# Optimization experiments

Hardware: AMD Instinct MI355X
Metric: run time of the kernel (lower is better)

The kernel has to match this reference:

```python
import jax, jax.numpy as jnp
import numpy as np

B = 131072   # batch
D = 16       # input_dim
L1 = 4       # num lattices in layer 1 (= ceil(D / DPL))
DPL = 4      # input_dim_per_lattice
E = 24       # output_size (ensemble columns)
K = 16       # calibrator keypoints per feature
NV = 2 ** DPL  # hypercube corners per lattice (lattice_keypoints=2 per dim)


def setup_inputs() -> dict:
    key = jax.random.key(0)
    k1, k2, k3, k4, k5 = jax.random.split(key, 5)
    x = jax.random.normal(k1, (B, D), jnp.float32)
    # piecewise-linear calibrators: sorted input keypoints, monotone outputs in [0,1]
    cal_kp = jnp.sort(jax.random.uniform(k2, (D, K), jnp.float32, -3.0, 3.0), axis=-1)
    raw = jax.random.uniform(k3, (D, K), jnp.float32, 0.1, 1.0)
    cv = jnp.cumsum(raw, axis=-1)
    cal_vals = (cv - cv[:, :1]) / (cv[:, -1:] - cv[:, :1])  # [D,K] in [0,1], increasing
    kernels1 = jax.random.uniform(k4, (E, L1, NV), jnp.float32)  # per-column layer-1 lattice vertices
    kernels2 = jax.random.uniform(k5, (E, 1, NV), jnp.float32)   # per-column layer-2 lattice vertices
    return {"x": x, "cal_kp": cal_kp, "cal_vals": cal_vals,
            "kernels1": kernels1, "kernels2": kernels2}


def _mlin_weights(xg):
    """Multilinear (HYPERCUBE) interpolation weights for unit lattices.
    xg: [..., L, d] with entries in [0,1]. Returns [..., L, 2^d] corner weights,
    corner index with dim 0 as most-significant bit."""
    d = xg.shape[-1]
    w = jnp.ones(xg.shape[:-1] + (1,), xg.dtype)
    for i in range(d):
        xi = xg[..., i]                              # [..., L]
        pair = jnp.stack([1.0 - xi, xi], axis=-1)    # [..., L, 2]
        w = (w[..., :, None] * pair[..., None, :]).reshape(*xg.shape[:-1], -1)
    return w


def reference(x, cal_kp, cal_vals, kernels1, kernels2):
    # 1) calibrate_and_stack: per-feature piecewise-linear calibration to [0,1]
    xc = jax.vmap(jnp.interp)(x.T, cal_kp, cal_vals).T           # [B, D]
    # 2) layer 1: split D dims into L1 lattices of DPL dims each (clip_inputs=True)
    xg1 = jnp.clip(xc.reshape(-1, L1, DPL), 0.0, 1.0)            # [B, L1, DPL]
    w1 = _mlin_weights(xg1)                                      # [B, L1, 2^DPL]
    h1 = jnp.einsum('blk,elk->ebl', w1, kernels1)                # [E, B, L1]
    # 3) layer 2: one lattice of DPL dims per ensemble column
    xg2 = jnp.clip(h1[:, :, None, :], 0.0, 1.0)                  # [E, B, 1, DPL]
    w2 = _mlin_weights(xg2)                                      # [E, B, 1, 2^DPL]
    out = jnp.einsum('eblk,elk->be', w2, kernels2)               # [B, E]
    return out
```

## Files before the change

### kernel.cpp

```cpp
#include <hip/hip_runtime.h>


typedef _Float16 f16x4 __attribute__((ext_vector_type(4)));
typedef float f32x4 __attribute__((ext_vector_type(4)));
typedef float f32x2 __attribute__((ext_vector_type(2)));

namespace {
constexpr int kD = 16, kE = 24, kK = 16, kNV = 16;
constexpr int kThreads = 256;
constexpr int kRPB = 64;
constexpr int kKpS  = 17;
constexpr int kAffS = 17;
constexpr int kWS   = 67;
constexpr int kK2S  = 20;
}

static __device__ __forceinline__ f32x2 fma2(f32x2 a, f32x2 b, f32x2 c) {
#if __has_builtin(__builtin_elementwise_fma)
    return __builtin_elementwise_fma(a, b, c);
#else
    return (f32x2){fmaf(a[0], b[0], c[0]), fmaf(a[1], b[1], c[1])};
#endif
}
static __device__ __forceinline__ f32x2 fma2s(f32x2 a, float b, float c) {
    return fma2(a, (f32x2){b, b}, (f32x2){c, c});
}
static __device__ __forceinline__ f32x2 clamp01(f32x2 v) {
    return (f32x2){fminf(fmaxf(v[0], 0.f), 1.f), fminf(fmaxf(v[1], 0.f), 1.f)};
}

__global__ __launch_bounds__(kThreads, 8) void lattice_fwd(
    const float* __restrict__ x,
    const float* __restrict__ cal_kp,
    const float* __restrict__ cal_vals,
    const float* __restrict__ k1,
    const float* __restrict__ k2,
    float* __restrict__ out)
{
    __shared__ float sKp[kD * kKpS];
    __shared__ f32x2 sAff[kD * kAffS];
    __shared__ f16x4 sW[16 * kWS];
    __shared__ f16x4 sK1[4 * 2 * 64];
    __shared__ float sK2[32 * kK2S];

    const int tid  = threadIdx.x;
    const int lane = tid & 63;
    const int wv   = __builtin_amdgcn_readfirstlane(tid >> 6);
    const int q    = lane >> 4;
    const int r15  = lane & 15;

    const int rowBase = blockIdx.x * kRPB + wv * 16;

    f32x4 xin = *reinterpret_cast<const f32x4*>(
        x + (size_t)(rowBase + r15) * kD + 4 * q);

    {
        int d = tid >> 4, k = tid & 15;
        sKp[d * kKpS + k] = (k == 15) ? __builtin_inff() : cal_kp[tid];
    }
    if (tid < kD * 15) {
        int d = tid / 15;
        int k = tid - d * 15;
        float kp0 = cal_kp[d * kK + k];
        float kp1 = cal_kp[d * kK + k + 1];
        float v0  = cal_vals[d * kK + k];
        float v1  = cal_vals[d * kK + k + 1];
        float dxv = kp1 - kp0;
        float slope = (dxv > 0.0f) ? (v1 - v0) / dxv : 0.0f;
        sAff[d * kAffS + k] = (f32x2){slope, fmaf(-slope, kp0, v0)};
    }
    #pragma unroll
    for (int s0 = 0; s0 < 2; ++s0) {
        int s  = tid + s0 * kThreads;
        int l  = s >> 7;
        int n  = (s >> 6) & 1;
        int ls = s & 63;
        int e  = n * 16 + (ls & 15);
        int g  = ls >> 4;
        f16x4 v = {(_Float16)0.f, (_Float16)0.f, (_Float16)0.f, (_Float16)0.f};
        if (e < kE) {
            const float* src = k1 + ((size_t)(e * 4 + l) * kNV + 4 * g);
            v[0] = (_Float16)src[0]; v[1] = (_Float16)src[1];
            v[2] = (_Float16)src[2]; v[3] = (_Float16)src[3];
        }
        sK1[s] = v;
    }
    {
        int e = tid >> 3, j4 = (tid >> 1) & 3, h = tid & 1;
        float a = 0.f, d = 0.f;
        if (e < kE) {
            a = k2[e * kNV + 4 * j4 + 2 * h];
            d = k2[e * kNV + 4 * j4 + 2 * h + 1] - a;
        }
        sK2[e * kK2S + 4 * j4 + h]     = a;
        sK2[e * kK2S + 4 * j4 + 2 + h] = d;
    }

    __syncthreads();

    float xc[4];
    #pragma unroll
    for (int i = 0; i < 4; ++i) {
        const int d = 4 * q + i;
        const float xv = xin[i];
        const float* kpb = &sKp[d * kKpS];
        int j = 0;
        #pragma unroll
        for (int s = 8; s >= 1; s >>= 1) {
            float kps = kpb[j + s];
            j = (xv >= kps) ? j + s : j;
        }
        f32x2 ent = sAff[d * kAffS + j];
        xc[i] = fminf(fmaxf(fmaf(ent[0], xv, ent[1]), 0.0f), 1.0f);
    }

    float wf[16];
    {
        float a = xc[0], b = xc[1], c = xc[2], d = xc[3];
        float t2[2] = {1.0f - a, a};
        float t4[4];
        #pragma unroll
        for (int j = 0; j < 2; ++j) { t4[2*j] = t2[j]*(1.0f-b); t4[2*j+1] = t2[j]*b; }
        float t8[8];
        #pragma unroll
        for (int j = 0; j < 4; ++j) { t8[2*j] = t4[j]*(1.0f-c); t8[2*j+1] = t4[j]*c; }
        #pragma unroll
        for (int j = 0; j < 8; ++j) { wf[2*j] = t8[j]*(1.0f-d); wf[2*j+1] = t8[j]*d; }
    }

    #pragma unroll
    for (int g = 0; g < 4; ++g) {
        f16x4 v;
        v[0] = (_Float16)wf[4*g+0]; v[1] = (_Float16)wf[4*g+1];
        v[2] = (_Float16)wf[4*g+2]; v[3] = (_Float16)wf[4*g+3];
        sW[(wv * 4 + q) * kWS + r15 + 16 * g] = v;
    }
    asm volatile("s_waitcnt lgkmcnt(0)" ::: "memory");

    f16x4 af[4];
    #pragma unroll
    for (int l = 0; l < 4; ++l) af[l] = sW[(wv * 4 + l) * kWS + lane];

    #pragma unroll
    for (int n = 0; n < 2; ++n) {
        const int e = n * 16 + r15;

        f32x4 acc[4];
        #pragma unroll
        for (int l = 0; l < 4; ++l) {
            f16x4 bf = sK1[(l * 2 + n) * 64 + lane];
            acc[l] = __builtin_amdgcn_mfma_f32_16x16x16f16(
                af[l], bf, (f32x4){0.f, 0.f, 0.f, 0.f}, 0, 0, 0);
        }

        f32x2 h3a = clamp01((f32x2){acc[3][0], acc[3][1]});
        f32x2 h3b = clamp01((f32x2){acc[3][2], acc[3][3]});
        f32x2 h2a = clamp01((f32x2){acc[2][0], acc[2][1]});
        f32x2 h2b = clamp01((f32x2){acc[2][2], acc[2][3]});

        f32x2 v4a[4], v4b[4];
        const float* kr = &sK2[e * kK2S];
        #pragma unroll
        for (int j4 = 0; j4 < 4; ++j4) {
            f32x4 kq = *reinterpret_cast<const f32x4*>(kr + 4 * j4);
            f32x2 a0 = fma2s(h3a, kq[2], kq[0]);
            f32x2 b0 = fma2s(h3a, kq[3], kq[1]);
            v4a[j4]  = fma2(h2a, b0 - a0, a0);
            f32x2 a1 = fma2s(h3b, kq[2], kq[0]);
            f32x2 b1 = fma2s(h3b, kq[3], kq[1]);
            v4b[j4]  = fma2(h2b, b1 - a1, a1);
        }

        #pragma unroll
        for (int p = 0; p < 2; ++p) {
            f32x2 h1 = clamp01((f32x2){acc[1][2*p], acc[1][2*p+1]});
            f32x2 h0 = clamp01((f32x2){acc[0][2*p], acc[0][2*p+1]});
            const f32x2* v4 = (p == 0) ? v4a : v4b;
            f32x2 w0 = fma2(h1, v4[1] - v4[0], v4[0]);
            f32x2 w1 = fma2(h1, v4[3] - v4[2], v4[2]);
            f32x2 o  = fma2(h0, w1 - w0, w0);
            if (e < kE) {
                size_t r0 = (size_t)(rowBase + q * 4 + 2 * p);
                out[r0 * kE + e]       = o[0];
                out[(r0 + 1) * kE + e] = o[1];
            }
        }
    }
}

extern "C" void kernel_launch(void* const* d_in, const int* in_sizes, int n_in,
                              void* d_out, int out_size, void* d_ws, size_t ws_size,
                              hipStream_t stream) {
    const float* x        = (const float*)d_in[0];
    const float* cal_kp   = (const float*)d_in[1];
    const float* cal_vals = (const float*)d_in[2];
    const float* k1       = (const float*)d_in[3];
    const float* k2       = (const float*)d_in[4];
    float* out = (float*)d_out;

    hipLaunchKernelGGL(lattice_fwd, dim3(131072 / kRPB), dim3(kThreads), 0, stream,
                       x, cal_kp, cal_vals, k1, k2, out);
}
```

Measured before the change: 14.13 us.

## Keep lattice kernels in registers and process two row tiles per block

Layer-1 MFMA B-fragments and the layer-2 vertex coefficients are now loaded straight from global memory into registers, replacing the shared-memory staging arrays. Each block also handles two 64-row tiles, prefetching the next tile's x before working on the current one, which halves the grid and amortizes the per-block setup of calibration tables. The cost is higher register pressure (launch bounds lowered to 4 waves) and fewer blocks for latency hiding.

```diff
diff --git a/kernel.cpp b/kernel.cpp
--- a/kernel.cpp
+++ b/kernel.cpp
@@ -8,11 +8,11 @@
 namespace {
 constexpr int kD = 16, kE = 24, kK = 16, kNV = 16;
 constexpr int kThreads = 256;
-constexpr int kRPB = 64;
+constexpr int kRPT = 64;
+constexpr int kTPB = 2;
 constexpr int kKpS  = 17;
 constexpr int kAffS = 17;
 constexpr int kWS   = 67;
-constexpr int kK2S  = 20;
 }
 
 static __device__ __forceinline__ f32x2 fma2(f32x2 a, f32x2 b, f32x2 c) {
@@ -29,7 +29,7 @@
     return (f32x2){fminf(fmaxf(v[0], 0.f), 1.f), fminf(fmaxf(v[1], 0.f), 1.f)};
 }
 
-__global__ __launch_bounds__(kThreads, 8) void lattice_fwd(
+__global__ __launch_bounds__(kThreads, 4) void lattice_fwd(
     const float* __restrict__ x,
     const float* __restrict__ cal_kp,
     const float* __restrict__ cal_vals,
@@ -40,19 +40,38 @@
     __shared__ float sKp[kD * kKpS];
     __shared__ f32x2 sAff[kD * kAffS];
     __shared__ f16x4 sW[16 * kWS];
-    __shared__ f16x4 sK1[4 * 2 * 64];
-    __shared__ float sK2[32 * kK2S];
 
     const int tid  = threadIdx.x;
     const int lane = tid & 63;
     const int wv   = __builtin_amdgcn_readfirstlane(tid >> 6);
     const int q    = lane >> 4;
     const int r15  = lane & 15;
-
-    const int rowBase = blockIdx.x * kRPB + wv * 16;
-
-    f32x4 xin = *reinterpret_cast<const f32x4*>(
-        x + (size_t)(rowBase + r15) * kD + 4 * q);
+    const int g    = lane >> 4;
+
+    const int eN[2]  = {r15, 16 + r15};
+    const int eLd[2] = {r15, (16 + r15 < kE) ? 16 + r15 : kE - 1};
+
+    f16x4 bf[4][2];
+    #pragma unroll
+    for (int l = 0; l < 4; ++l)
+        #pragma unroll
+        for (int n = 0; n < 2; ++n) {
+            f32x4 v = *reinterpret_cast<const f32x4*>(
+                k1 + ((size_t)(eLd[n] * 4 + l) * kNV + 4 * g));
+            f16x4 h;
+            h[0] = (_Float16)v[0]; h[1] = (_Float16)v[1];
+            h[2] = (_Float16)v[2]; h[3] = (_Float16)v[3];
+            bf[l][n] = h;
+        }
+    f32x4 kq[2][4];
+    #pragma unroll
+    for (int n = 0; n < 2; ++n)
+        #pragma unroll
+        for (int j4 = 0; j4 < 4; ++j4) {
+            f32x4 c = *reinterpret_cast<const f32x4*>(
+                k2 + (size_t)eLd[n] * kNV + 4 * j4);
+            kq[n][j4] = (f32x4){c[0], c[2], c[1] - c[0], c[3] - c[2]};
+        }
 
     {
         int d = tid >> 4, k = tid & 15;
@@ -69,120 +88,102 @@
         float slope = (dxv > 0.0f) ? (v1 - v0) / dxv : 0.0f;
         sAff[d * kAffS + k] = (f32x2){slope, fmaf(-slope, kp0, v0)};
     }
-    #pragma unroll
-    for (int s0 = 0; s0 < 2; ++s0) {
-        int s  = tid + s0 * kThreads;
-        int l  = s >> 7;
-        int n  = (s >> 6) & 1;
-        int ls = s & 63;
-        int e  = n * 16 + (ls & 15);
-        int g  = ls >> 4;
-        f16x4 v = {(_Float16)0.f, (_Float16)0.f, (_Float16)0.f, (_Float16)0.f};
-        if (e < kE) {
-            const float* src = k1 + ((size_t)(e * 4 + l) * kNV + 4 * g);
-            v[0] = (_Float16)src[0]; v[1] = (_Float16)src[1];
-            v[2] = (_Float16)src[2]; v[3] = (_Float16)src[3];
-        }
-        sK1[s] = v;
-    }
-    {
-        int e = tid >> 3, j4 = (tid >> 1) & 3, h = tid & 1;
-        float a = 0.f, d = 0.f;
-        if (e < kE) {
-            a = k2[e * kNV + 4 * j4 + 2 * h];
-            d = k2[e * kNV + 4 * j4 + 2 * h + 1] - a;
-        }
-        sK2[e * kK2S + 4 * j4 + h]     = a;
-        sK2[e * kK2S + 4 * j4 + 2 + h] = d;
-    }
 
     __syncthreads();
 
-    float xc[4];
-    #pragma unroll
-    for (int i = 0; i < 4; ++i) {
-        const int d = 4 * q + i;
-        const float xv = xin[i];
-        const float* kpb = &sKp[d * kKpS];
-        int j = 0;
-        #pragma unroll
-        for (int s = 8; s >= 1; s >>= 1) {
-            float kps = kpb[j + s];
-            j = (xv >= kps) ? j + s : j;
-        }
-        f32x2 ent = sAff[d * kAffS + j];
-        xc[i] = fminf(fmaxf(fmaf(ent[0], xv, ent[1]), 0.0f), 1.0f);
-    }
-
-    float wf[16];
-    {
-        float a = xc[0], b = xc[1], c = xc[2], d = xc[3];
-        float t2[2] = {1.0f - a, a};
-        float t4[4];
-        #pragma unroll
-        for (int j = 0; j < 2; ++j) { t4[2*j] = t2[j]*(1.0f-b); t4[2*j+1] = t2[j]*b; }
-        float t8[8];
-        #pragma unroll
-        for (int j = 0; j < 4; ++j) { t8[2*j] = t4[j]*(1.0f-c); t8[2*j+1] = t4[j]*c; }
-        #pragma unroll
-        for (int j = 0; j < 8; ++j) { wf[2*j] = t8[j]*(1.0f-d); wf[2*j+1] = t8[j]*d; }
-    }
-
-    #pragma unroll
-    for (int g = 0; g < 4; ++g) {
-        f16x4 v;
-        v[0] = (_Float16)wf[4*g+0]; v[1] = (_Float16)wf[4*g+1];
-        v[2] = (_Float16)wf[4*g+2]; v[3] = (_Float16)wf[4*g+3];
-        sW[(wv * 4 + q) * kWS + r15 + 16 * g] = v;
-    }
-    asm volatile("s_waitcnt lgkmcnt(0)" ::: "memory");
-
-    f16x4 af[4];
-    #pragma unroll
-    for (int l = 0; l < 4; ++l) af[l] = sW[(wv * 4 + l) * kWS + lane];
-
-    #pragma unroll
-    for (int n = 0; n < 2; ++n) {
-        const int e = n * 16 + r15;
-
-        f32x4 acc[4];
-        #pragma unroll
-        for (int l = 0; l < 4; ++l) {
-            f16x4 bf = sK1[(l * 2 + n) * 64 + lane];
-            acc[l] = __builtin_amdgcn_mfma_f32_16x16x16f16(
-                af[l], bf, (f32x4){0.f, 0.f, 0.f, 0.f}, 0, 0, 0);
-        }
-
-        f32x2 h3a = clamp01((f32x2){acc[3][0], acc[3][1]});
-        f32x2 h3b = clamp01((f32x2){acc[3][2], acc[3][3]});
-        f32x2 h2a = clamp01((f32x2){acc[2][0], acc[2][1]});
-        f32x2 h2b = clamp01((f32x2){acc[2][2], acc[2][3]});
-
-        f32x2 v4a[4], v4b[4];
-        const float* kr = &sK2[e * kK2S];
-        #pragma unroll
-        for (int j4 = 0; j4 < 4; ++j4) {
-            f32x4 kq = *reinterpret_cast<const f32x4*>(kr + 4 * j4);
-            f32x2 a0 = fma2s(h3a, kq[2], kq[0]);
-            f32x2 b0 = fma2s(h3a, kq[3], kq[1]);
-            v4a[j4]  = fma2(h2a, b0 - a0, a0);
-            f32x2 a1 = fma2s(h3b, kq[2], kq[0]);
-            f32x2 b1 = fma2s(h3b, kq[3], kq[1]);
-            v4b[j4]  = fma2(h2b, b1 - a1, a1);
-        }
-
-        #pragma unroll
-        for (int p = 0; p < 2; ++p) {
-            f32x2 h1 = clamp01((f32x2){acc[1][2*p], acc[1][2*p+1]});
-            f32x2 h0 = clamp01((f32x2){acc[0][2*p], acc[0][2*p+1]});
-            const f32x2* v4 = (p == 0) ? v4a : v4b;
-            f32x2 w0 = fma2(h1, v4[1] - v4[0], v4[0]);
-            f32x2 w1 = fma2(h1, v4[3] - v4[2], v4[2]);
-            f32x2 o  = fma2(h0, w1 - w0, w0);
-            if (e < kE) {
-                size_t r0 = (size_t)(rowBase + q * 4 + 2 * p);
-                out[r0 * kE + e]       = o[0];
-                out[(r0 + 1) * kE + e] = o[1];
+    const int rowTile0 = blockIdx.x * (kRPT * kTPB);
+    f32x4 xin = *reinterpret_cast<const f32x4*>(
+        x + (size_t)(rowTile0 + wv * 16 + r15) * kD + 4 * q);
+
+    for (int t = 0; t < kTPB; ++t) {
+        const int rowBase = rowTile0 + t * kRPT + wv * 16;
+        f32x4 xcur = xin;
+        if (t + 1 < kTPB)
+            xin = *reinterpret_cast<const f32x4*>(
+                x + (size_t)(rowTile0 + (t + 1) * kRPT + wv * 16 + r15) * kD + 4 * q);
+
+        float xc[4];
+        #pragma unroll
+        for (int i = 0; i < 4; ++i) {
+            const int d = 4 * q + i;
+            const float xv = xcur[i];
+            const float* kpb = &sKp[d * kKpS];
+            int j = 0;
+            #pragma unroll
+            for (int s = 8; s >= 1; s >>= 1) {
+                float kps = kpb[j + s];
+                j = (xv >= kps) ? j + s : j;
+            }
+            f32x2 ent = sAff[d * kAffS + j];
+            xc[i] = fminf(fmaxf(fmaf(ent[0], xv, ent[1]), 0.0f), 1.0f);
+        }
+
+        float wf[16];
+        {
+            float a = xc[0], b = xc[1], c = xc[2], d = xc[3];
+            float t2[2] = {1.0f - a, a};
+            float t4[4];
+            #pragma unroll
+            for (int j = 0; j < 2; ++j) { t4[2*j] = t2[j]*(1.0f-b); t4[2*j+1] = t2[j]*b; }
+            float t8[8];
+            #pragma unroll
+            for (int j = 0; j < 4; ++j) { t8[2*j] = t4[j]*(1.0f-c); t8[2*j+1] = t4[j]*c; }
+            #pragma unroll
+            for (int j = 0; j < 8; ++j) { wf[2*j] = t8[j]*(1.0f-d); wf[2*j+1] = t8[j]*d; }
+        }
+
+        #pragma unroll
+        for (int gg = 0; gg < 4; ++gg) {
+            f16x4 v;
+            v[0] = (_Float16)wf[4*gg+0]; v[1] = (_Float16)wf[4*gg+1];
+            v[2] = (_Float16)wf[4*gg+2]; v[3] = (_Float16)wf[4*gg+3];
+            sW[(wv * 4 + q) * kWS + r15 + 16 * gg] = v;
+        }
+        asm volatile("s_waitcnt lgkmcnt(0)" ::: "memory");
+
+        f16x4 af[4];
+        #pragma unroll
+        for (int l = 0; l < 4; ++l) af[l] = sW[(wv * 4 + l) * kWS + lane];
+
+        #pragma unroll
+        for (int n = 0; n < 2; ++n) {
+            f32x4 acc[4];
+            #pragma unroll
+            for (int l = 0; l < 4; ++l)
+                acc[l] = __builtin_amdgcn_mfma_f32_16x16x16f16(
+                    af[l], bf[l][n], (f32x4){0.f, 0.f, 0.f, 0.f}, 0, 0, 0);
+
+            f32x2 h3a = clamp01((f32x2){acc[3][0], acc[3][1]});
+            f32x2 h3b = clamp01((f32x2){acc[3][2], acc[3][3]});
+            f32x2 h2a = clamp01((f32x2){acc[2][0], acc[2][1]});
+            f32x2 h2b = clamp01((f32x2){acc[2][2], acc[2][3]});
+
+            f32x2 v4a[4], v4b[4];
+            #pragma unroll
+            for (int j4 = 0; j4 < 4; ++j4) {
+                f32x4 kv = kq[n][j4];
+                f32x2 a0 = fma2s(h3a, kv[2], kv[0]);
+                f32x2 b0 = fma2s(h3a, kv[3], kv[1]);
+                v4a[j4]  = fma2(h2a, b0 - a0, a0);
+                f32x2 a1 = fma2s(h3b, kv[2], kv[0]);
+                f32x2 b1 = fma2s(h3b, kv[3], kv[1]);
+                v4b[j4]  = fma2(h2b, b1 - a1, a1);
+            }
+
+            const int e = eN[n];
+            #pragma unroll
+            for (int p = 0; p < 2; ++p) {
+                f32x2 h1 = clamp01((f32x2){acc[1][2*p], acc[1][2*p+1]});
+                f32x2 h0 = clamp01((f32x2){acc[0][2*p], acc[0][2*p+1]});
+                const f32x2* v4 = (p == 0) ? v4a : v4b;
+                f32x2 w0 = fma2(h1, v4[1] - v4[0], v4[0]);
+                f32x2 w1 = fma2(h1, v4[3] - v4[2], v4[2]);
+                f32x2 o  = fma2(h0, w1 - w0, w0);
+                if (e < kE) {
+                    size_t r0 = (size_t)(rowBase + q * 4 + 2 * p);
+                    out[r0 * kE + e]       = o[0];
+                    out[(r0 + 1) * kE + e] = o[1];
+                }
             }
         }
     }
@@ -198,6 +199,6 @@
     const float* k2       = (const float*)d_in[4];
     float* out = (float*)d_out;
 
-    hipLaunchKernelGGL(lattice_fwd, dim3(131072 / kRPB), dim3(kThreads), 0, stream,
-                       x, cal_kp, cal_vals, k1, k2, out);
-}
+    hipLaunchKernelGGL(lattice_fwd, dim3(131072 / (kRPT * kTPB)), dim3(kThreads),
+                       0, stream, x, cal_kp, cal_vals, k1, k2, out);
+}
```

Measured after the change: 16.63 us. 17.7% more time.
